# Optimization experiments

Hardware: AMD Instinct MI355X
Metric: run time of the kernel (lower is better)

Reference implementation:

```python
import jax, jax.numpy as jnp
import numpy as np

N = 2000      # num_of_vertices
T = 12        # history
B = 4         # batch
C = 32        # in_dim == out_dims[i]
STRIDES = 3
L = 3         # len(out_dims)
W_WIN = T - STRIDES + 1  # 10 sliding windows


def setup_inputs() -> dict:
    key = jax.random.key(0)
    ks = jax.random.split(key, 12)
    adj_scale = 2.0 / (3 * N)  # keep row sums ~1 so activations stay in range
    fc_scale = 1.0 / np.sqrt(C)
    g_scale = 1.0 / np.sqrt(2 * C)
    return {
        "x": jax.random.normal(ks[0], (B, T, N, C), jnp.float32),
        "adj": jax.random.uniform(ks[1], (3 * N, 3 * N), jnp.float32) * adj_scale,
        "temporal_adj": jax.random.uniform(ks[2], (N, N), jnp.float32) * adj_scale,
        "temporal_embedding": jax.random.normal(ks[3], (1, T, 1, C), jnp.float32) * 0.0003,
        "spatial_embedding": jax.random.normal(ks[4], (1, 1, N, C), jnp.float32) * 0.0003,
        "W_fc": jax.random.normal(ks[5], (W_WIN, L, C, 2 * C), jnp.float32) * fc_scale,
        "b_fc": jnp.zeros((W_WIN, L, 2 * C), jnp.float32),
        "Wr": jax.random.normal(ks[6], (2 * C, C), jnp.float32) * g_scale,
        "br": jnp.zeros((C,), jnp.float32),
        "Wu": jax.random.normal(ks[7], (2 * C, C), jnp.float32) * g_scale,
        "bu": jnp.zeros((C,), jnp.float32),
        "Wn": jax.random.normal(ks[8], (2 * C, C), jnp.float32) * g_scale,
        "bn": jnp.zeros((C,), jnp.float32),
        "Wo": jax.random.normal(ks[9], (C, C), jnp.float32) * (1.0 / np.sqrt(C)),
        "bo": jnp.zeros((C,), jnp.float32),
    }


def _forward(x, adj, temporal_adj, temporal_embedding, spatial_embedding,
             W_fc, b_fc, Wr, br, Wu, bu, Wn, bn, Wo, bo):
    # x: (B, T, N, C)
    x = x + temporal_embedding + spatial_embedding

    # Patch the 3Nx3N adjacency: 4 corner N x N blocks become temporal_adj
    A = adj.at[:N, :N].set(temporal_adj)
    A = A.at[2 * N:, 2 * N:].set(temporal_adj)
    A = A.at[2 * N:, :N].set(temporal_adj)
    A = A.at[:N, 2 * N:].set(temporal_adj)

    # Extract all sliding windows at once: (B, W, 3, N, C)
    idx = jnp.arange(W_WIN)[:, None] + jnp.arange(STRIDES)[None, :]
    xw = x[:, idx]
    # -> (W, 3N, B, C) matching torch reshape(B, 3*N, C).permute(1,0,2)
    h = jnp.transpose(xw, (1, 2, 3, 0, 4)).reshape(W_WIN, STRIDES * N, B, C)

    # STSGCM stack (per-window weights), GLU activation
    layer_mid = []
    for l in range(L):
        h = jnp.einsum('nm,wmbc->wnbc', A, h)                 # graph conv
        z = jnp.einsum('wnbc,wcd->wnbd', h, W_fc[:, l]) + b_fc[:, l][:, None, None, :]
        lhs, rhs = jnp.split(z, 2, axis=-1)
        h = lhs * jax.nn.sigmoid(rhs)                         # GLU
        layer_mid.append(h[:, N:2 * N])                       # middle time slice (W, N, B, C)
    out = jnp.max(jnp.stack(layer_mid, axis=0), axis=0)      # max over layers
    out = jnp.transpose(out, (2, 0, 1, 3))                    # (B, W, N, C)

    # GRU-style gating across the W time slices (note: next hidden is yt)
    def step(hid, inp):
        comb = jnp.concatenate([inp, hid], axis=-1)
        reset = jax.nn.sigmoid(comb @ Wr + br)
        update = jax.nn.sigmoid(comb @ Wu + bu)
        comb_new = jnp.concatenate([inp, reset * hid], axis=-1)
        new_mem = jnp.tanh(comb_new @ Wn + bn)
        output = update * hid + (1.0 - update) * new_mem
        yt = jax.nn.sigmoid(output @ Wo + bo)
        return yt, output

    h0 = jnp.zeros((B, N, C), x.dtype)
    _, residual = jax.lax.scan(step, h0, jnp.transpose(out, (1, 0, 2, 3)))
    residual = jnp.transpose(residual, (1, 0, 2, 3))          # (B, W, N, C)
    return out + residual


def reference(x, adj, temporal_adj, temporal_embedding, spatial_embedding,
              W_fc, b_fc, Wr, br, Wu, bu, Wn, bn, Wo, bo):
    return _forward(x, adj, temporal_adj, temporal_embedding, spatial_embedding,
                    W_fc, b_fc, Wr, br, Wu, bu, Wn, bn, Wo, bo)
```

## Files before the change

### kernel.cpp

```cpp
#include <hip/hip_runtime.h>
#include <hip/hip_bf16.h>

#define N_NODE 2000
#define BB 4
#define CC 32
#define LL 3
#define WW 10
#define M3 6000
#define MP 6016
#define KP 6016
#define NCOL 1280

typedef __bf16 bf16x8 __attribute__((ext_vector_type(8)));
typedef float f32x4 __attribute__((ext_vector_type(4)));
typedef unsigned short ushort8 __attribute__((ext_vector_type(8)));

__device__ __forceinline__ float sigmoidf_(float x) { return 1.0f / (1.0f + __expf(-x)); }
__device__ __forceinline__ float tanhf_(float x) { return 1.0f - 2.0f / (__expf(2.0f * x) + 1.0f); }

__global__ __launch_bounds__(256) void k_build_A(const float* __restrict__ adj,
                                                 const float* __restrict__ tadj,
                                                 __hip_bfloat16* __restrict__ A) {
  const int m8 = blockIdx.x * 256 + threadIdx.x;
  const int m = m8 * 8;
  const int n = blockIdx.y;
  if (m >= KP) return;
  ushort8 out = {0, 0, 0, 0, 0, 0, 0, 0};
  if (n < M3 && m < M3) {
    const bool nr = (n < N_NODE) | (n >= 2 * N_NODE);
    const bool mr = (m < N_NODE) | (m >= 2 * N_NODE);
    const float* src;
    if (nr & mr) {
      const int nn = (n >= 2 * N_NODE) ? n - 2 * N_NODE : n;
      const int mm = (m >= 2 * N_NODE) ? m - 2 * N_NODE : m;
      src = tadj + (size_t)nn * N_NODE + mm;
    } else {
      src = adj + (size_t)n * M3 + m;
    }
#pragma unroll
    for (int j = 0; j < 8; ++j) {
      union { __hip_bfloat16 h; unsigned short u; } cv;
      cv.h = __float2bfloat16(src[j]);
      out[j] = cv.u;
    }
  }
  *(ushort8*)(A + (size_t)n * KP + m) = out;
}

__global__ __launch_bounds__(256) void k_build_H(const float* __restrict__ x,
                                                 const float* __restrict__ temb,
                                                 const float* __restrict__ semb,
                                                 __hip_bfloat16* __restrict__ H) {
  const int m = blockIdx.x * 256 + threadIdx.x;
  const int col = blockIdx.y;
  if (m >= KP) return;
  float v = 0.0f;
  if (m < M3) {
    const int w = col >> 7, b = (col >> 5) & 3, c = col & 31;
    const int s = (m >= 2 * N_NODE) ? 2 : (m >= N_NODE ? 1 : 0);
    const int n = m - s * N_NODE;
    const int tt = w + s;
    v = x[(((size_t)b * 12 + tt) * N_NODE + n) * CC + c] + temb[tt * CC + c] +
        semb[(size_t)n * CC + c];
  }
  H[(size_t)col * KP + m] = __float2bfloat16(v);
}

__global__ __launch_bounds__(256) void k_gemm(const __hip_bfloat16* __restrict__ A,
                                              const __hip_bfloat16* __restrict__ Bt,
                                              float* __restrict__ G) {
  __shared__ __align__(16) char lA[128 * 128];
  __shared__ __align__(16) char lB[128 * 128];
  const int tid = threadIdx.x;
  const int lane = tid & 63;
  const int wv = tid >> 6;
  const int wr = wv >> 1, wc = wv & 1;

  const int bid = blockIdx.x + 47 * blockIdx.y;
  const int q = 470 / 8, r = 470 % 8;
  const int xcd = bid & 7, lid = bid >> 3;
  const int swz = (xcd < r ? xcd * (q + 1) : r * (q + 1) + (xcd - r) * q) + lid;
  const int bx = swz % 47;
  const int by = swz / 47;
  const long row0 = (long)bx * 128;
  const long col0 = (long)by * 128;

  const int srow = wv * 32 + (lane >> 3);
  const int soff = ((lane & 7) ^ (lane >> 3)) << 4;
  const char* gA = (const char*)A + (size_t)(row0 + srow) * (KP * 2) + soff;
  const char* gB = (const char*)Bt + (size_t)(col0 + srow) * (KP * 2) + soff;
  const size_t rstep = (size_t)8 * KP * 2;

  const int rrow = lane & 15;
  const int off0 = (((lane >> 4) << 4)) ^ ((lane & 7) << 4);
  const int off1 = (64 | ((lane >> 4) << 4)) ^ ((lane & 7) << 4);

  f32x4 acc[4][4] = {};

  const int NKT = KP / 64;
  for (int kt = 0; kt < NKT; ++kt) {
    __syncthreads();
    const char* ga = gA + (size_t)kt * 128;
    const char* gb = gB + (size_t)kt * 128;
#pragma unroll
    for (int i = 0; i < 4; ++i) {
      __builtin_amdgcn_global_load_lds(
          (const __attribute__((address_space(1))) void*)(ga + (size_t)i * rstep),
          (__attribute__((address_space(3))) void*)(lA + wv * 4096 + i * 1024), 16, 0, 0);
    }
#pragma unroll
    for (int i = 0; i < 4; ++i) {
      __builtin_amdgcn_global_load_lds(
          (const __attribute__((address_space(1))) void*)(gb + (size_t)i * rstep),
          (__attribute__((address_space(3))) void*)(lB + wv * 4096 + i * 1024), 16, 0, 0);
    }
    __syncthreads();
#pragma unroll
    for (int ks = 0; ks < 2; ++ks) {
      const int offk = ks ? off1 : off0;
      bf16x8 af[4], bfr[4];
#pragma unroll
      for (int mi = 0; mi < 4; ++mi)
        af[mi] = *(const bf16x8*)(lA + (wr * 64 + mi * 16 + rrow) * 128 + offk);
#pragma unroll
      for (int ni = 0; ni < 4; ++ni)
        bfr[ni] = *(const bf16x8*)(lB + (wc * 64 + ni * 16 + rrow) * 128 + offk);
#pragma unroll
      for (int mi = 0; mi < 4; ++mi)
#pragma unroll
        for (int ni = 0; ni < 4; ++ni)
          acc[mi][ni] =
              __builtin_amdgcn_mfma_f32_16x16x32_bf16(af[mi], bfr[ni], acc[mi][ni], 0, 0, 0);
    }
  }
  const int crow = (lane >> 4) * 4;
  const int ccol = lane & 15;
#pragma unroll
  for (int mi = 0; mi < 4; ++mi) {
#pragma unroll
    for (int ni = 0; ni < 4; ++ni) {
      const long r_ = row0 + wr * 64 + mi * 16 + crow;
      const long cix = col0 + wc * 64 + ni * 16 + ccol;
      float* gp = G + (size_t)r_ * NCOL + cix;
#pragma unroll
      for (int j = 0; j < 4; ++j) gp[(size_t)j * NCOL] = acc[mi][ni][j];
    }
  }
}

__global__ __launch_bounds__(256) void k_fcglu(const float* __restrict__ G,
                                               const float* __restrict__ Wfc,
                                               const float* __restrict__ bfc,
                                               __hip_bfloat16* __restrict__ Hn,
                                               float* __restrict__ outb, int l, int writeH) {
  __shared__ float sW[32 * 64];
  __shared__ float sb[64];
  const int w = blockIdx.y;
  const int t = threadIdx.x;
  const float* Ws = Wfc + (size_t)(w * LL + l) * 32 * 64;
#pragma unroll
  for (int i = 0; i < 8; ++i) sW[t + 256 * i] = Ws[t + 256 * i];
  if (t < 64) sb[t] = bfc[(size_t)(w * LL + l) * 64 + t];
  __syncthreads();
  const int nl = t >> 2, b = t & 3;
  const int n = blockIdx.x * 64 + nl;
  const int colbase = w * 128 + b * 32;
  if (n >= M3) {
    if (writeH) {
      for (int c = 0; c < 32; ++c) Hn[(size_t)(colbase + c) * KP + n] = __float2bfloat16(0.0f);
    }
    return;
  }
  const float* g = G + (size_t)n * NCOL + colbase;
  float z[64];
#pragma unroll
  for (int d = 0; d < 64; ++d) z[d] = sb[d];
  for (int c = 0; c < 32; ++c) {
    const float gv = g[c];
#pragma unroll
    for (int d = 0; d < 64; ++d) z[d] = fmaf(gv, sW[c * 64 + d], z[d]);
  }
  float h[32];
#pragma unroll
  for (int c = 0; c < 32; ++c) h[c] = z[c] * sigmoidf_(z[32 + c]);
  if (writeH) {
#pragma unroll
    for (int c = 0; c < 32; ++c) Hn[(size_t)(colbase + c) * KP + n] = __float2bfloat16(h[c]);
  }
  if (n >= N_NODE && n < 2 * N_NODE) {
    float* op = outb + (((size_t)b * WW + w) * N_NODE + (n - N_NODE)) * CC;
    if (l == 0) {
#pragma unroll
      for (int c = 0; c < 32; ++c) op[c] = h[c];
    } else {
#pragma unroll
      for (int c = 0; c < 32; ++c) op[c] = fmaxf(op[c], h[c]);
    }
  }
}

__global__ __launch_bounds__(256) void k_gru(float* __restrict__ outb, float* __restrict__ state,
                                             const float* __restrict__ Wr,
                                             const float* __restrict__ brr,
                                             const float* __restrict__ Wu,
                                             const float* __restrict__ bu,
                                             const float* __restrict__ Wn,
                                             const float* __restrict__ bnn,
                                             const float* __restrict__ Wo,
                                             const float* __restrict__ bo, int w) {
  __shared__ float sI[8][32], sH[8][32], sT[8][32];
  const int t = threadIdx.x;
  const int g = t >> 5, c = t & 31;
  const int n = blockIdx.x * 8 + g;
  const int b = blockIdx.y;
  const size_t oix = (((size_t)b * WW + w) * N_NODE + n) * CC + c;
  const size_t hix = ((size_t)b * N_NODE + n) * CC + c;
  const float inp = outb[oix];
  const float hid = state[hix];
  sI[g][c] = inp;
  sH[g][c] = hid;
  __syncthreads();
  float ar = brr[c], au = bu[c];
#pragma unroll 4
  for (int d = 0; d < 32; ++d) {
    const float i_ = sI[g][d], h_ = sH[g][d];
    ar = fmaf(i_, Wr[d * 32 + c], ar);
    ar = fmaf(h_, Wr[(32 + d) * 32 + c], ar);
    au = fmaf(i_, Wu[d * 32 + c], au);
    au = fmaf(h_, Wu[(32 + d) * 32 + c], au);
  }
  const float r = sigmoidf_(ar), u = sigmoidf_(au);
  sT[g][c] = r * hid;
  __syncthreads();
  float an = bnn[c];
#pragma unroll 4
  for (int d = 0; d < 32; ++d) {
    an = fmaf(sI[g][d], Wn[d * 32 + c], an);
    an = fmaf(sT[g][d], Wn[(32 + d) * 32 + c], an);
  }
  const float nm = tanhf_(an);
  const float outv = u * hid + (1.0f - u) * nm;
  __syncthreads();
  sT[g][c] = outv;
  __syncthreads();
  float ay = bo[c];
#pragma unroll 4
  for (int d = 0; d < 32; ++d) ay = fmaf(sT[g][d], Wo[d * 32 + c], ay);
  state[hix] = sigmoidf_(ay);
  outb[oix] = inp + outv;
}

extern "C" void kernel_launch(void* const* d_in, const int* in_sizes, int n_in, void* d_out,
                              int out_size, void* d_ws, size_t ws_size, hipStream_t stream) {
  const float* x = (const float*)d_in[0];
  const float* adj = (const float*)d_in[1];
  const float* tadj = (const float*)d_in[2];
  const float* temb = (const float*)d_in[3];
  const float* semb = (const float*)d_in[4];
  const float* Wfc = (const float*)d_in[5];
  const float* bfc = (const float*)d_in[6];
  const float* Wr = (const float*)d_in[7];
  const float* brr = (const float*)d_in[8];
  const float* Wu = (const float*)d_in[9];
  const float* bu = (const float*)d_in[10];
  const float* Wn = (const float*)d_in[11];
  const float* bnn = (const float*)d_in[12];
  const float* Wo = (const float*)d_in[13];
  const float* bo = (const float*)d_in[14];
  float* outb = (float*)d_out;

  char* ws = (char*)d_ws;
  const size_t szA = (size_t)MP * KP * 2;
  const size_t szH = (size_t)NCOL * KP * 2;
  const size_t szG = (size_t)MP * NCOL * 4;
  const size_t szS = (size_t)BB * N_NODE * CC * 4;
  if (ws_size < szA + 2 * szH + szG + szS) return;

  __hip_bfloat16* A = (__hip_bfloat16*)ws;
  __hip_bfloat16* H0 = (__hip_bfloat16*)(ws + szA);
  __hip_bfloat16* H1 = (__hip_bfloat16*)(ws + szA + szH);
  float* G = (float*)(ws + szA + 2 * szH);
  float* state = (float*)(ws + szA + 2 * szH + szG);

  hipMemsetAsync(state, 0, szS, stream);
  k_build_A<<<dim3(3, KP), 256, 0, stream>>>(adj, tadj, A);
  k_build_H<<<dim3(24, NCOL), 256, 0, stream>>>(x, temb, semb, H0);

  __hip_bfloat16* Hc = H0;
  __hip_bfloat16* Hx = H1;
  for (int l = 0; l < LL; ++l) {
    k_gemm<<<dim3(47, 10), 256, 0, stream>>>(A, Hc, G);
    k_fcglu<<<dim3(94, 10), 256, 0, stream>>>(G, Wfc, bfc, Hx, outb, l, l < 2 ? 1 : 0);
    __hip_bfloat16* tmp = Hc;
    Hc = Hx;
    Hx = tmp;
  }
  for (int w = 0; w < WW; ++w)
    k_gru<<<dim3(250, BB), 256, 0, stream>>>(outb, state, Wr, brr, Wu, bu, Wn, bnn, Wo, bo, w);
}
```

Before: 882.2 us.

## Split-K the adjacency GEMM with atomics and fuse GRU steps into one kernel

The GEMM grid gains a z dimension that splits the K loop into two halves of 47 tiles each. Partial sums are accumulated into G with atomicAdd, so G is zeroed before every layer. This raises the block count from 470 to 940 to fill more CUs, at the cost of a memset per layer and atomic traffic on G. The ten per-timestep GRU launches are replaced by one kernel that keeps the hidden state in registers and the weights in LDS, which removes the state buffer, its memset and the repeated launches.

```diff
diff --git a/kernel.cpp b/kernel.cpp
--- a/kernel.cpp
+++ b/kernel.cpp
@@ -76,12 +76,14 @@
   const int wv = tid >> 6;
   const int wr = wv >> 1, wc = wv & 1;
 
-  const int bid = blockIdx.x + 47 * blockIdx.y;
-  const int q = 470 / 8, r = 470 % 8;
+  const int bid = blockIdx.x + 47 * (blockIdx.y + 10 * blockIdx.z);
+  const int q = 940 / 8, r = 940 % 8;
   const int xcd = bid & 7, lid = bid >> 3;
   const int swz = (xcd < r ? xcd * (q + 1) : r * (q + 1) + (xcd - r) * q) + lid;
   const int bx = swz % 47;
-  const int by = swz / 47;
+  const int tmp = swz / 47;
+  const int by = tmp % 10;
+  const int kt0 = (tmp / 10) * 47;
   const long row0 = (long)bx * 128;
   const long col0 = (long)by * 128;
 
@@ -97,8 +99,7 @@
 
   f32x4 acc[4][4] = {};
 
-  const int NKT = KP / 64;
-  for (int kt = 0; kt < NKT; ++kt) {
+  for (int kt = kt0; kt < kt0 + 47; ++kt) {
     __syncthreads();
     const char* ga = gA + (size_t)kt * 128;
     const char* gb = gB + (size_t)kt * 128;
@@ -143,7 +144,7 @@
       const long cix = col0 + wc * 64 + ni * 16 + ccol;
       float* gp = G + (size_t)r_ * NCOL + cix;
 #pragma unroll
-      for (int j = 0; j < 4; ++j) gp[(size_t)j * NCOL] = acc[mi][ni][j];
+      for (int j = 0; j < 4; ++j) atomicAdd(gp + (size_t)j * NCOL, acc[mi][ni][j]);
     }
   }
 }
@@ -199,55 +200,73 @@
   }
 }
 
-__global__ __launch_bounds__(256) void k_gru(float* __restrict__ outb, float* __restrict__ state,
-                                             const float* __restrict__ Wr,
-                                             const float* __restrict__ brr,
-                                             const float* __restrict__ Wu,
-                                             const float* __restrict__ bu,
-                                             const float* __restrict__ Wn,
-                                             const float* __restrict__ bnn,
-                                             const float* __restrict__ Wo,
-                                             const float* __restrict__ bo, int w) {
+__global__ __launch_bounds__(256) void k_gru_all(float* __restrict__ outb,
+                                                 const float* __restrict__ Wr,
+                                                 const float* __restrict__ brr,
+                                                 const float* __restrict__ Wu,
+                                                 const float* __restrict__ bu,
+                                                 const float* __restrict__ Wn,
+                                                 const float* __restrict__ bnn,
+                                                 const float* __restrict__ Wo,
+                                                 const float* __restrict__ bo) {
+  __shared__ float sWr[2048], sWu[2048], sWn[2048], sWo[1024];
+  __shared__ float sbr[32], sbu[32], sbn[32], sbo[32];
   __shared__ float sI[8][32], sH[8][32], sT[8][32];
   const int t = threadIdx.x;
+  for (int i = t; i < 2048; i += 256) {
+    sWr[i] = Wr[i];
+    sWu[i] = Wu[i];
+    sWn[i] = Wn[i];
+  }
+  for (int i = t; i < 1024; i += 256) sWo[i] = Wo[i];
+  if (t < 32) {
+    sbr[t] = brr[t];
+    sbu[t] = bu[t];
+    sbn[t] = bnn[t];
+    sbo[t] = bo[t];
+  }
+  __syncthreads();
   const int g = t >> 5, c = t & 31;
   const int n = blockIdx.x * 8 + g;
   const int b = blockIdx.y;
-  const size_t oix = (((size_t)b * WW + w) * N_NODE + n) * CC + c;
-  const size_t hix = ((size_t)b * N_NODE + n) * CC + c;
-  const float inp = outb[oix];
-  const float hid = state[hix];
-  sI[g][c] = inp;
-  sH[g][c] = hid;
-  __syncthreads();
-  float ar = brr[c], au = bu[c];
+  float hid = 0.0f;
+  for (int w = 0; w < WW; ++w) {
+    const size_t oix = (((size_t)b * WW + w) * N_NODE + n) * CC + c;
+    const float inp = outb[oix];
+    sI[g][c] = inp;
+    sH[g][c] = hid;
+    __syncthreads();
+    float ar = sbr[c], au = sbu[c];
 #pragma unroll 4
-  for (int d = 0; d < 32; ++d) {
-    const float i_ = sI[g][d], h_ = sH[g][d];
-    ar = fmaf(i_, Wr[d * 32 + c], ar);
-    ar = fmaf(h_, Wr[(32 + d) * 32 + c], ar);
-    au = fmaf(i_, Wu[d * 32 + c], au);
-    au = fmaf(h_, Wu[(32 + d) * 32 + c], au);
-  }
-  const float r = sigmoidf_(ar), u = sigmoidf_(au);
-  sT[g][c] = r * hid;
-  __syncthreads();
-  float an = bnn[c];
+    for (int d = 0; d < 32; ++d) {
+      const float i_ = sI[g][d], h_ = sH[g][d];
+      ar = fmaf(i_, sWr[d * 32 + c], ar);
+      ar = fmaf(h_, sWr[(32 + d) * 32 + c], ar);
+      au = fmaf(i_, sWu[d * 32 + c], au);
+      au = fmaf(h_, sWu[(32 + d) * 32 + c], au);
+    }
+    const float r = sigmoidf_(ar), u = sigmoidf_(au);
+    __syncthreads();
+    sT[g][c] = r * hid;
+    __syncthreads();
+    float an = sbn[c];
 #pragma unroll 4
-  for (int d = 0; d < 32; ++d) {
-    an = fmaf(sI[g][d], Wn[d * 32 + c], an);
-    an = fmaf(sT[g][d], Wn[(32 + d) * 32 + c], an);
-  }
-  const float nm = tanhf_(an);
-  const float outv = u * hid + (1.0f - u) * nm;
-  __syncthreads();
-  sT[g][c] = outv;
-  __syncthreads();
-  float ay = bo[c];
+    for (int d = 0; d < 32; ++d) {
+      an = fmaf(sI[g][d], sWn[d * 32 + c], an);
+      an = fmaf(sT[g][d], sWn[(32 + d) * 32 + c], an);
+    }
+    const float nm = tanhf_(an);
+    const float outv = u * hid + (1.0f - u) * nm;
+    __syncthreads();
+    sT[g][c] = outv;
+    __syncthreads();
+    float ay = sbo[c];
 #pragma unroll 4
-  for (int d = 0; d < 32; ++d) ay = fmaf(sT[g][d], Wo[d * 32 + c], ay);
-  state[hix] = sigmoidf_(ay);
-  outb[oix] = inp + outv;
+    for (int d = 0; d < 32; ++d) ay = fmaf(sT[g][d], sWo[d * 32 + c], ay);
+    hid = sigmoidf_(ay);
+    outb[oix] = inp + outv;
+    __syncthreads();
+  }
 }
 
 extern "C" void kernel_launch(void* const* d_in, const int* in_sizes, int n_in, void* d_out,
@@ -273,28 +292,25 @@
   const size_t szA = (size_t)MP * KP * 2;
   const size_t szH = (size_t)NCOL * KP * 2;
   const size_t szG = (size_t)MP * NCOL * 4;
-  const size_t szS = (size_t)BB * N_NODE * CC * 4;
-  if (ws_size < szA + 2 * szH + szG + szS) return;
+  if (ws_size < szA + 2 * szH + szG) return;
 
   __hip_bfloat16* A = (__hip_bfloat16*)ws;
   __hip_bfloat16* H0 = (__hip_bfloat16*)(ws + szA);
   __hip_bfloat16* H1 = (__hip_bfloat16*)(ws + szA + szH);
   float* G = (float*)(ws + szA + 2 * szH);
-  float* state = (float*)(ws + szA + 2 * szH + szG);
-
-  hipMemsetAsync(state, 0, szS, stream);
+
   k_build_A<<<dim3(3, KP), 256, 0, stream>>>(adj, tadj, A);
   k_build_H<<<dim3(24, NCOL), 256, 0, stream>>>(x, temb, semb, H0);
 
   __hip_bfloat16* Hc = H0;
   __hip_bfloat16* Hx = H1;
   for (int l = 0; l < LL; ++l) {
-    k_gemm<<<dim3(47, 10), 256, 0, stream>>>(A, Hc, G);
+    hipMemsetAsync(G, 0, szG, stream);
+    k_gemm<<<dim3(47, 10, 2), 256, 0, stream>>>(A, Hc, G);
     k_fcglu<<<dim3(94, 10), 256, 0, stream>>>(G, Wfc, bfc, Hx, outb, l, l < 2 ? 1 : 0);
     __hip_bfloat16* tmp = Hc;
     Hc = Hx;
     Hx = tmp;
   }
-  for (int w = 0; w < WW; ++w)
-    k_gru<<<dim3(250, BB), 256, 0, stream>>>(outb, state, Wr, brr, Wu, bu, Wn, bnn, Wo, bo, w);
-}
+  k_gru_all<<<dim3(250, BB), 256, 0, stream>>>(outb, Wr, brr, Wu, bu, Wn, bnn, Wo, bo);
+}
```

Measured after the change: 945.7 us. +7.2%, slower.
